# Kernel tuning notes

Hardware: AMD Instinct MI355X
Metric: run time of the kernel (lower is better)

Reference implementation:

```python
import jax, jax.numpy as jnp
import numpy as np

NUM_EXPERTS = 64
HIDDEN = 4096
TOP_K = 2
B, S = 4, 4096


def setup_inputs() -> dict:
    key = jax.random.key(0)
    k1, k2 = jax.random.split(key)
    hidden_states = jax.random.normal(k1, (B, S, HIDDEN), dtype=jnp.float32)
    W = jax.random.normal(k2, (NUM_EXPERTS, HIDDEN), dtype=jnp.float32) * 0.02
    return {"hidden_states": hidden_states, "W": W}


def reference(hidden_states, W):
    # router logits: [B, S, E]
    logits = jnp.einsum("bsh,eh->bse", hidden_states, W)
    flat = logits.reshape(-1, NUM_EXPERTS)  # [T, E]
    # top-k routing (z-loss / aux-loss do not change forward values; they only
    # inject gradients via the custom autograd function in the torch original)
    scores, top_indices = jax.lax.top_k(flat, TOP_K)  # [T, K] each
    return (scores.reshape(B, S, TOP_K), top_indices.reshape(B, S, TOP_K))
```

## Files before the change

kernel.cpp:

```cpp
#include <hip/hip_runtime.h>
#include <hip/hip_bf16.h>
#include <math.h>

#define NUM_EXPERTS 64
#define HIDDEN      4096
#define T_TOKENS    16384

using short8 = __attribute__((ext_vector_type(8))) short;
using f32x4  = __attribute__((ext_vector_type(4))) float;

__device__ __forceinline__ unsigned pack_pair(float f0, float f1, unsigned& lopk) {
    __hip_bfloat162 h2 = __float22bfloat162_rn(make_float2(f0, f1));
    unsigned hb; __builtin_memcpy(&hb, &h2, 4);
    float h0 = __builtin_bit_cast(float, hb << 16);
    float h1 = __builtin_bit_cast(float, hb & 0xffff0000u);
    __hip_bfloat162 l2 = __float22bfloat162_rn(make_float2(f0 - h0, f1 - h1));
    unsigned lb; __builtin_memcpy(&lb, &l2, 4);
    lopk = lb;
    return hb;
}
__device__ __forceinline__ void split8(const float4 a, const float4 b, uint4& hi, uint4& lo) {
    hi.x = pack_pair(a.x, a.y, lo.x);
    hi.y = pack_pair(a.z, a.w, lo.y);
    hi.z = pack_pair(b.x, b.y, lo.z);
    hi.w = pack_pair(b.z, b.w, lo.w);
}

#define MFMA(a, b, c) __builtin_amdgcn_mfma_f32_16x16x32_bf16((a), (b), (c), 0, 0, 0)

#define GLOAD16(g_, l_)                                                        \
    __builtin_amdgcn_global_load_lds(                                          \
        (__attribute__((address_space(1))) unsigned*)(void*)(g_),              \
        (__attribute__((address_space(3))) unsigned*)(void*)(l_), 16, 0, 0)

__global__ __launch_bounds__(256) void w_split_kernel(
    const float* __restrict__ W, unsigned char* __restrict__ ws)
{
    const int j  = blockIdx.x * 256 + threadIdx.x;
    const int l  = j & 63;
    const int nt = (j >> 6) & 3;
    const int t  = j >> 8;
    const int e  = nt * 16 + (l & 15);
    const int k0 = t * 32 + ((l >> 4) & 3) * 8;
    const float* p = W + (size_t)e * HIDDEN + k0;
    float4 w0 = *reinterpret_cast<const float4*>(p);
    float4 w1 = *reinterpret_cast<const float4*>(p + 4);
    uint4 hi, lo;
    split8(w0, w1, hi, lo);
    *reinterpret_cast<uint4*>(ws + (size_t)j * 16)            = hi;
    *reinterpret_cast<uint4*>(ws + 524288 + (size_t)j * 16)   = lo;
}


#define LOAD_W(dst, t_) do {                                                   \
    const unsigned char* pW_ = wsHi + (size_t)(tBase + (t_)) * 4096 + laneOff; \
    _Pragma("unroll")                                                          \
    for (int nt_ = 0; nt_ < 4; ++nt_) {                                        \
        dst[nt_]     = *reinterpret_cast<const uint4*>(pW_ + nt_ * 1024);      \
        dst[nt_ + 4] = *reinterpret_cast<const uint4*>(pW_ + 524288 + nt_ * 1024); \
    } } while (0)

#define STAGE_A(b_, t_) do {                                                   \
    unsigned char* ld_ = smem + (size_t)w * 16384 + (b_) * 8192;               \
    const float* g0_ = aBase + (size_t)(t_) * 32;                              \
    _Pragma("unroll")                                                          \
    for (int mt_ = 0; mt_ < 4; ++mt_) {                                        \
        const float* g_ = g0_ + (size_t)mt_ * 16 * HIDDEN;                     \
        GLOAD16(g_,     ld_ + mt_ * 2048);                                     \
        GLOAD16(g_ + 4, ld_ + mt_ * 2048 + 1024);                              \
    } } while (0)

#define CHUNK_LDS(b_, wb_) do {                                                \
    const unsigned char* ls_ = smem + (size_t)w * 16384 + (b_) * 8192 + laneOff; \
    _Pragma("unroll")                                                          \
    for (int mt_ = 0; mt_ < 4; ++mt_) {                                        \
        float4 q0_ = *reinterpret_cast<const float4*>(ls_ + mt_ * 2048);       \
        float4 q1_ = *reinterpret_cast<const float4*>(ls_ + mt_ * 2048 + 1024);\
        uint4 hi_, lo_;                                                        \
        split8(q0_, q1_, hi_, lo_);                                            \
        short8 ah_ = __builtin_bit_cast(short8, hi_);                          \
        short8 al_ = __builtin_bit_cast(short8, lo_);                          \
        _Pragma("unroll")                                                      \
        for (int nt_ = 0; nt_ < 4; ++nt_) {                                    \
            short8 wh_ = __builtin_bit_cast(short8, wb_[nt_]);                 \
            short8 wl_ = __builtin_bit_cast(short8, wb_[nt_ + 4]);             \
            acc[mt_][nt_] = MFMA(ah_, wh_, acc[mt_][nt_]);                     \
            acc[mt_][nt_] = MFMA(ah_, wl_, acc[mt_][nt_]);                     \
            acc[mt_][nt_] = MFMA(al_, wh_, acc[mt_][nt_]);                     \
        } } } while (0)

__global__ __launch_bounds__(512, 2) void router_mfma_topk(
    const float* __restrict__ A,
    const unsigned char* __restrict__ wsHi,
    float* __restrict__ out)
{
    __shared__ unsigned char smem[131072];

    const int tid  = threadIdx.x;
    const int lane = tid & 63;
    const int w    = tid >> 6;
    const int tok0 = blockIdx.x * 64;
    const int tBase = w * 16;

    const float* aBase = A + (size_t)(tok0 + (lane & 15)) * HIDDEN
                           + w * 512 + ((lane >> 4) & 3) * 8;
    const int laneOff = lane * 16;

    f32x4 acc[4][4];
#pragma unroll
    for (int mt = 0; mt < 4; ++mt)
#pragma unroll
        for (int nt = 0; nt < 4; ++nt) acc[mt][nt] = (f32x4){0.f, 0.f, 0.f, 0.f};

    uint4 wX[8], wY[8];

    LOAD_W(wX, 0);
    STAGE_A(0, 0);
    __syncthreads();

    for (int tt = 0; tt < 8; ++tt) {
        const int t = tt * 2;
        LOAD_W(wY, t + 1);
        STAGE_A(1, t + 1);
        CHUNK_LDS(0, wX);
        __syncthreads();
        if (tt < 7) { LOAD_W(wX, t + 2); STAGE_A(0, t + 2); }
        CHUNK_LDS(1, wY);
        __syncthreads();
    }

    f32x4 (*part)[4][4][64] = reinterpret_cast<f32x4 (*)[4][4][64]>(smem);

    if (w < 4) {
#pragma unroll
        for (int mt = 0; mt < 4; ++mt)
#pragma unroll
            for (int nt = 0; nt < 4; ++nt) part[w][mt][nt][lane] = acc[mt][nt];
    }
    __syncthreads();
    if (w >= 4) {
#pragma unroll
        for (int mt = 0; mt < 4; ++mt)
#pragma unroll
            for (int nt = 0; nt < 4; ++nt)
                part[w - 4][mt][nt][lane] = part[w - 4][mt][nt][lane] + acc[mt][nt];
    }
    __syncthreads();

    if (w < 4) {
        f32x4 s[4];
#pragma unroll
        for (int nt = 0; nt < 4; ++nt) {
            s[nt] = part[0][w][nt][lane];
#pragma unroll
            for (int q = 1; q < 4; ++q) s[nt] = s[nt] + part[q][w][nt][lane];
        }

        const int eBase = lane & 15;
#pragma unroll
        for (int r = 0; r < 4; ++r) {
            float b1 = s[0][r]; int i1 = eBase;
            float b2 = -INFINITY; int i2 = 0;
#pragma unroll
            for (int nt = 1; nt < 4; ++nt) {
                float v = s[nt][r];
                int   e = nt * 16 + eBase;
                if (v > b1)      { b2 = b1; i2 = i1; b1 = v; i1 = e; }
                else if (v > b2) { b2 = v;  i2 = e; }
            }
#pragma unroll
            for (int m = 1; m <= 8; m <<= 1) {
                float o1 = __shfl_xor(b1, m); int oi1 = __shfl_xor(i1, m);
                float o2 = __shfl_xor(b2, m); int oi2 = __shfl_xor(i2, m);
                float n1, c, n2; int ni1, ci, ni2;
                if (o1 > b1 || (o1 == b1 && oi1 < i1)) { n1 = o1; ni1 = oi1; c = b1; ci = i1; }
                else                                   { n1 = b1; ni1 = i1;  c = o1; ci = oi1; }
                if (b2 > o2 || (b2 == o2 && i2 < oi2)) { n2 = b2; ni2 = i2; }
                else                                   { n2 = o2; ni2 = oi2; }
                if (c > n2 || (c == n2 && ci < ni2))   { n2 = c;  ni2 = ci; }
                b1 = n1; i1 = ni1; b2 = n2; i2 = ni2;
            }
            if ((lane & 15) == 0) {
                const int tok = tok0 + w * 16 + (lane >> 4) * 4 + r;
                out[(size_t)tok * 2 + 0] = b1;
                out[(size_t)tok * 2 + 1] = b2;
                out[(size_t)2 * T_TOKENS + (size_t)tok * 2 + 0] = (float)i1;
                out[(size_t)2 * T_TOKENS + (size_t)tok * 2 + 1] = (float)i2;
            }
        }
    }
}

extern "C" void kernel_launch(void* const* d_in, const int* in_sizes, int n_in,
                              void* d_out, int out_size, void* d_ws, size_t ws_size,
                              hipStream_t stream) {
    const float* A = (const float*)d_in[0];
    const float* W = (const float*)d_in[1];
    float* out = (float*)d_out;
    unsigned char* ws = (unsigned char*)d_ws;

    w_split_kernel<<<dim3(128), dim3(256), 0, stream>>>(W, ws);
    router_mfma_topk<<<dim3(T_TOKENS / 64), dim3(512), 0, stream>>>(A, ws, out);
}
```

Baseline: 75.30 us.

## Replace block barriers with per-wave waitcnt pipelining and deeper A prefetch

```diff
diff --git a/kernel.cpp b/kernel.cpp
--- a/kernel.cpp
+++ b/kernel.cpp
@@ -70,24 +70,35 @@
         GLOAD16(g_ + 4, ld_ + mt_ * 2048 + 1024);                              \
     } } while (0)
 
-#define CHUNK_LDS(b_, wb_) do {                                                \
-    const unsigned char* ls_ = smem + (size_t)w * 16384 + (b_) * 8192 + laneOff; \
+#define ITER(t_, bufA_, wCur_, wNxt_) do {                                     \
+    asm volatile("s_waitcnt vmcnt(8)" ::: "memory");                           \
+    __builtin_amdgcn_sched_barrier(0);                                         \
+    const unsigned char* ls_ = smem + (size_t)w * 16384 + (bufA_) * 8192 + laneOff; \
+    float4 q_[4][2];                                                           \
     _Pragma("unroll")                                                          \
     for (int mt_ = 0; mt_ < 4; ++mt_) {                                        \
-        float4 q0_ = *reinterpret_cast<const float4*>(ls_ + mt_ * 2048);       \
-        float4 q1_ = *reinterpret_cast<const float4*>(ls_ + mt_ * 2048 + 1024);\
+        q_[mt_][0] = *reinterpret_cast<const float4*>(ls_ + mt_ * 2048);       \
+        q_[mt_][1] = *reinterpret_cast<const float4*>(ls_ + mt_ * 2048 + 1024);\
+    }                                                                          \
+    asm volatile("s_waitcnt lgkmcnt(0)" ::: "memory");                         \
+    __builtin_amdgcn_sched_barrier(0);                                         \
+    if ((t_) + 1 < 16) LOAD_W(wNxt_, (t_) + 1);                                \
+    if ((t_) + 2 < 16) STAGE_A(bufA_, (t_) + 2);                               \
+    _Pragma("unroll")                                                          \
+    for (int mt_ = 0; mt_ < 4; ++mt_) {                                        \
         uint4 hi_, lo_;                                                        \
-        split8(q0_, q1_, hi_, lo_);                                            \
+        split8(q_[mt_][0], q_[mt_][1], hi_, lo_);                              \
         short8 ah_ = __builtin_bit_cast(short8, hi_);                          \
         short8 al_ = __builtin_bit_cast(short8, lo_);                          \
         _Pragma("unroll")                                                      \
         for (int nt_ = 0; nt_ < 4; ++nt_) {                                    \
-            short8 wh_ = __builtin_bit_cast(short8, wb_[nt_]);                 \
-            short8 wl_ = __builtin_bit_cast(short8, wb_[nt_ + 4]);             \
+            short8 wh_ = __builtin_bit_cast(short8, wCur_[nt_]);               \
+            short8 wl_ = __builtin_bit_cast(short8, wCur_[nt_ + 4]);           \
             acc[mt_][nt_] = MFMA(ah_, wh_, acc[mt_][nt_]);                     \
             acc[mt_][nt_] = MFMA(ah_, wl_, acc[mt_][nt_]);                     \
             acc[mt_][nt_] = MFMA(al_, wh_, acc[mt_][nt_]);                     \
-        } } } while (0)
+        } }                                                                    \
+} while (0)
 
 __global__ __launch_bounds__(512, 2) void router_mfma_topk(
     const float* __restrict__ A,
@@ -116,21 +127,20 @@
 
     LOAD_W(wX, 0);
     STAGE_A(0, 0);
+    STAGE_A(1, 1);
+
+    ITER( 0, 0, wX, wY);  ITER( 1, 1, wY, wX);
+    ITER( 2, 0, wX, wY);  ITER( 3, 1, wY, wX);
+    ITER( 4, 0, wX, wY);  ITER( 5, 1, wY, wX);
+    ITER( 6, 0, wX, wY);  ITER( 7, 1, wY, wX);
+    ITER( 8, 0, wX, wY);  ITER( 9, 1, wY, wX);
+    ITER(10, 0, wX, wY);  ITER(11, 1, wY, wX);
+    ITER(12, 0, wX, wY);  ITER(13, 1, wY, wX);
+    ITER(14, 0, wX, wY);  ITER(15, 1, wY, wX);
+
+    f32x4 (*part)[4][4][64] = reinterpret_cast<f32x4 (*)[4][4][64]>(smem);
+
     __syncthreads();
-
-    for (int tt = 0; tt < 8; ++tt) {
-        const int t = tt * 2;
-        LOAD_W(wY, t + 1);
-        STAGE_A(1, t + 1);
-        CHUNK_LDS(0, wX);
-        __syncthreads();
-        if (tt < 7) { LOAD_W(wX, t + 2); STAGE_A(0, t + 2); }
-        CHUNK_LDS(1, wY);
-        __syncthreads();
-    }
-
-    f32x4 (*part)[4][4][64] = reinterpret_cast<f32x4 (*)[4][4][64]>(smem);
-
     if (w < 4) {
 #pragma unroll
         for (int mt = 0; mt < 4; ++mt)
```

Result: faster. 64.19 us (-14.7%).
